# Optimization experiments

Measured on AMD Instinct MI355X. Metric: run time of the kernel, lower is better.

Reference implementation:

```python
import jax, jax.numpy as jnp
import numpy as np

B, S, D, H = 4, 2048, 1024, 16
DH = D // H  # 64
NEG_INF = jnp.float32(-1e30)


def setup_inputs() -> dict:
    key = jax.random.key(0)
    ks = jax.random.split(key, 11)
    s = 0.02
    inp = {
        "query": jax.random.normal(ks[0], (B, S, D), jnp.float32),
        "key":   jax.random.normal(ks[1], (B, S, D), jnp.float32),
        "value": jax.random.normal(ks[2], (B, S, D), jnp.float32),
        # causal mask, broadcastable to [B,H,Sq,Sk]; 0 -> masked
        "mask": jnp.tril(jnp.ones((S, S), jnp.int32))[None, None, :, :],
        "Wq": jax.random.normal(ks[3], (D, D), jnp.float32) * s,
        "bq": jnp.zeros((D,), jnp.float32),
        "Wk": jax.random.normal(ks[4], (D, D), jnp.float32) * s,
        "bk": jnp.zeros((D,), jnp.float32),
        "Wv": jax.random.normal(ks[5], (D, D), jnp.float32) * s,
        "bv": jnp.zeros((D,), jnp.float32),
        "Wo": jax.random.normal(ks[6], (D, D), jnp.float32) * s,
        "bo": jnp.zeros((D,), jnp.float32),
    }
    return inp


def _heads(x):
    # [B,S,D] -> [B,H,S,DH]
    b, s, _ = x.shape
    return x.reshape(b, s, H, DH).transpose(0, 2, 1, 3)


def reference(query, key, value, mask, Wq, bq, Wk, bk, Wv, bv, Wo, bo):
    q = _heads(query @ Wq.T + bq)   # [B,H,S,DH]
    k = _heads(key   @ Wk.T + bk)
    v = _heads(value @ Wv.T + bv)
    scale = 1.0 / jnp.sqrt(jnp.float32(DH))
    logits = jnp.einsum('bhqd,bhkd->bhqk', q, k) * scale  # [B,H,S,S]
    logits = jnp.where(mask == 0, NEG_INF, logits)
    attn = jax.nn.softmax(logits, axis=-1)
    out = jnp.einsum('bhqk,bhkd->bhqd', attn, v)          # [B,H,S,DH]
    out = out.transpose(0, 2, 1, 3).reshape(query.shape[0], query.shape[1], D)
    return out @ Wo.T + bo
```

## Files before the change

### kernel.cpp

```cpp
#include <hip/hip_runtime.h>
#include <hip/hip_bf16.h>
#include <stdint.h>

#define BB 4
#define SS 2048
#define DD 1024
#define HH 16
#define DHH 64

typedef __attribute__((ext_vector_type(8))) short short8_t;
typedef __attribute__((ext_vector_type(4))) short short4_t;
typedef __attribute__((ext_vector_type(4))) float f32x4;
typedef unsigned short u16;

static __device__ __forceinline__ u16 f2bf(float x) {
    uint32_t u = __float_as_uint(x);
    u += 0x7fffu + ((u >> 16) & 1u);
    return (u16)(u >> 16);
}

static __device__ __forceinline__ void gload16(const void* g, void* l) {
    __builtin_amdgcn_global_load_lds((const __attribute__((address_space(1))) void*)g,
                                     (__attribute__((address_space(3))) void*)l, 16, 0, 0);
}

__global__ __launch_bounds__(256) void convert_x3(
    const float* __restrict__ a, const float* __restrict__ b, const float* __restrict__ c,
    u16* __restrict__ oa, u16* __restrict__ ob, u16* __restrict__ oc)
{
    const float* s; u16* d;
    if (blockIdx.z == 0)      { s = a; d = oa; }
    else if (blockIdx.z == 1) { s = b; d = ob; }
    else                      { s = c; d = oc; }
    size_t i = ((size_t)blockIdx.x * 256 + threadIdx.x) * 8;
    f32x4 v0 = *(const f32x4*)(s + i);
    f32x4 v1 = *(const f32x4*)(s + i + 4);
    short8_t o;
#pragma unroll
    for (int j = 0; j < 4; j++) { o[j] = (short)f2bf(v0[j]); o[4 + j] = (short)f2bf(v1[j]); }
    *(short8_t*)(d + i) = o;
}

__global__ __launch_bounds__(256) void convert_w4(
    const float* __restrict__ a, const float* __restrict__ b,
    const float* __restrict__ c, const float* __restrict__ dd_,
    u16* __restrict__ oa, u16* __restrict__ ob, u16* __restrict__ oc, u16* __restrict__ od)
{
    const float* s; u16* d;
    if (blockIdx.z == 0)      { s = a;   d = oa; }
    else if (blockIdx.z == 1) { s = b;   d = ob; }
    else if (blockIdx.z == 2) { s = c;   d = oc; }
    else                      { s = dd_; d = od; }
    size_t i = ((size_t)blockIdx.x * 256 + threadIdx.x) * 8;
    f32x4 v0 = *(const f32x4*)(s + i);
    f32x4 v1 = *(const f32x4*)(s + i + 4);
    short8_t o;
#pragma unroll
    for (int j = 0; j < 4; j++) { o[j] = (short)f2bf(v0[j]); o[4 + j] = (short)f2bf(v1[j]); }
    *(short8_t*)(d + i) = o;
}

template<int OMODE>
__global__ __launch_bounds__(256) void gemm_v3(
    const u16* __restrict__ A, const u16* __restrict__ B,
    const float* __restrict__ bias, void* __restrict__ outp)
{
    __shared__ u16 As[128 * 64];
    __shared__ u16 Bs[128 * 64];

    const int tid = threadIdx.x;
    const int lane = tid & 63;
    const int w  = tid >> 6;
    const int wr = w >> 1, wc = w & 1;
    const int g  = lane >> 4, c = lane & 15;
    const int cs7 = c & 7;

    const int m0 = blockIdx.x * 128;
    const int n0 = blockIdx.y * 128;

    f32x4 acc[4][4] = {};

    const int srow  = w * 32 + (lane >> 3);
    const int sslot = (lane & 7) ^ (srow & 7);
    const u16* aSrc = A + (size_t)(m0 + srow) * DD + sslot * 8;
    const u16* bSrc = B + (size_t)(n0 + srow) * DD + sslot * 8;

    for (int ks = 0; ks < 16; ks++) {
        __syncthreads();
#pragma unroll
        for (int j = 0; j < 4; j++) {
            gload16(aSrc + (size_t)j * 8 * DD + ks * 64, &As[(w * 32 + j * 8) * 64]);
            gload16(bSrc + (size_t)j * 8 * DD + ks * 64, &Bs[(w * 32 + j * 8) * 64]);
        }
        __syncthreads();

#pragma unroll
        for (int kc = 0; kc < 2; kc++) {
            const int rdoff = ((kc * 4 + g) ^ cs7) * 8;
            short8_t af[4], bfr[4];
#pragma unroll
            for (int m = 0; m < 4; m++)
                af[m] = *(const short8_t*)&As[(wr * 64 + m * 16 + c) * 64 + rdoff];
#pragma unroll
            for (int n = 0; n < 4; n++)
                bfr[n] = *(const short8_t*)&Bs[(wc * 64 + n * 16 + c) * 64 + rdoff];
#pragma unroll
            for (int m = 0; m < 4; m++)
#pragma unroll
                for (int n = 0; n < 4; n++)
                    acc[m][n] = __builtin_amdgcn_mfma_f32_16x16x32_bf16(af[m], bfr[n], acc[m][n], 0, 0, 0);
        }
    }

    if (OMODE == 0) {
        u16* out = (u16*)outp;
#pragma unroll
        for (int m = 0; m < 4; m++)
#pragma unroll
            for (int n = 0; n < 4; n++) {
                const int gn = n0 + wc * 64 + n * 16 + c;
                const int h = gn >> 6, dh = gn & 63;
                const float bv_ = bias[gn];
#pragma unroll
                for (int i = 0; i < 4; i++) {
                    const int gm = m0 + wr * 64 + m * 16 + g * 4 + i;
                    const int b = gm >> 11, s = gm & (SS - 1);
                    out[(((size_t)(b * HH + h)) * SS + s) * DHH + dh] = f2bf(acc[m][n][i] + bv_);
                }
            }
    } else if (OMODE == 1) {
        u16* out = (u16*)outp;
#pragma unroll
        for (int m = 0; m < 4; m++)
#pragma unroll
            for (int n = 0; n < 4; n++) {
                const int gn = n0 + wc * 64 + n * 16 + c;
                const int h = gn >> 6, dh = gn & 63;
                const float bv_ = bias[gn];
                const int gm0 = m0 + wr * 64 + m * 16 + g * 4;
                const int b = gm0 >> 11, s = gm0 & (SS - 1);
                short4_t pk;
#pragma unroll
                for (int i = 0; i < 4; i++) pk[i] = (short)f2bf(acc[m][n][i] + bv_);
                *(short4_t*)&out[(((size_t)(b * HH + h)) * DHH + dh) * SS + s] = pk;
            }
    } else {
        float* out = (float*)outp;
#pragma unroll
        for (int m = 0; m < 4; m++)
#pragma unroll
            for (int n = 0; n < 4; n++) {
                const int gn = n0 + wc * 64 + n * 16 + c;
                const float bv_ = bias[gn];
#pragma unroll
                for (int i = 0; i < 4; i++) {
                    const int gm = m0 + wr * 64 + m * 16 + g * 4 + i;
                    out[(size_t)gm * DD + gn] = acc[m][n][i] + bv_;
                }
            }
    }
}

__global__ __launch_bounds__(256) void attn_v3(
    const u16* __restrict__ qb, const u16* __restrict__ kb,
    const u16* __restrict__ vtb, u16* __restrict__ attb)
{
    __shared__ u16 Kt[64 * 64];
    __shared__ u16 Vt[64 * 64];
    __shared__ u16 Pb[4][32 * 64];

    const int tid = threadIdx.x;
    const int lane = tid & 63;
    const int w = tid >> 6;
    const int g = lane >> 4, c = lane & 15;
    const int cs7 = c & 7;
    const int qt = 15 - blockIdx.x;
    const int bh = blockIdx.y;
    const size_t base = (size_t)bh * SS * DHH;
    const int qw = qt * 128 + w * 32;

    short8_t qa[2][2];
#pragma unroll
    for (int fr = 0; fr < 2; fr++)
#pragma unroll
        for (int kc = 0; kc < 2; kc++)
            qa[fr][kc] = *(const short8_t*)(qb + base + (size_t)(qw + fr * 16 + c) * DHH + kc * 32 + g * 8);

    f32x4 o[2][4] = {};
    float lp[2] = {0.f, 0.f};

    const int NT = 2 * qt + 2;
    const int sr = tid >> 2;
    const int s4 = (tid & 3) * 16;
    const int swz = (sr & 7) << 3;
    const u16* kpb = kb  + base + (size_t)sr * DHH + s4;
    const u16* vpb = vtb + base + (size_t)sr * SS + s4;

    short8_t kr0 = *(const short8_t*)(kpb);
    short8_t kr1 = *(const short8_t*)(kpb + 8);
    short8_t vr0 = *(const short8_t*)(vpb);
    short8_t vr1 = *(const short8_t*)(vpb + 8);

    for (int t = 0; t < NT; ++t) {
        __syncthreads();
        *(short8_t*)&Kt[sr * 64 + (s4 ^ swz)]       = kr0;
        *(short8_t*)&Kt[sr * 64 + ((s4 + 8) ^ swz)] = kr1;
        *(short8_t*)&Vt[sr * 64 + (s4 ^ swz)]       = vr0;
        *(short8_t*)&Vt[sr * 64 + ((s4 + 8) ^ swz)] = vr1;
        __syncthreads();

        if (t + 1 < NT) {
            kr0 = *(const short8_t*)(kpb + (size_t)(t + 1) * 64 * DHH);
            kr1 = *(const short8_t*)(kpb + (size_t)(t + 1) * 64 * DHH + 8);
            vr0 = *(const short8_t*)(vpb + (t + 1) * 64);
            vr1 = *(const short8_t*)(vpb + (t + 1) * 64 + 8);
        }

        const int k0g = t * 64;
        const bool act0 = (k0g <= qw + 15);
        const bool act1 = (k0g <= qw + 31);

        f32x4 sacc[2][4] = {};
#pragma unroll
        for (int n = 0; n < 4; n++) {
            const int krow = n * 16 + c;
            const int ksw = (krow & 7) << 3;
#pragma unroll
            for (int kc = 0; kc < 2; kc++) {
                short8_t kf = *(const short8_t*)&Kt[krow * 64 + ((kc * 32 + g * 8) ^ ksw)];
                if (act0) sacc[0][n] = __builtin_amdgcn_mfma_f32_16x16x32_bf16(kf, qa[0][kc], sacc[0][n], 0, 0, 0);
                if (act1) sacc[1][n] = __builtin_amdgcn_mfma_f32_16x16x32_bf16(kf, qa[1][kc], sacc[1][n], 0, 0, 0);
            }
        }

        const bool diag = (k0g + 63 > qw);
#pragma unroll
        for (int fr = 0; fr < 2; fr++) {
            if (fr == 0 ? !act0 : !act1) continue;
            const int qq = qw + fr * 16 + c;
            float e[4][4];
            float ls = 0.f;
#pragma unroll
            for (int n = 0; n < 4; n++) {
                const int kbse = k0g + n * 16 + 4 * g;
#pragma unroll
                for (int i = 0; i < 4; i++) {
                    float pv = exp2f(sacc[fr][n][i] * 0.18033688f);
                    if (diag && (kbse + i > qq)) pv = 0.f;
                    e[n][i] = pv;
                    ls += pv;
                }
            }
            lp[fr] += ls;
            const int prow = (fr * 16 + c) * 64;
#pragma unroll
            for (int n = 0; n < 4; n++)
#pragma unroll
                for (int hi = 0; hi < 2; hi++) {
                    uint32_t pk = (__float_as_uint(e[n][2 * hi]) >> 16) |
                                  (__float_as_uint(e[n][2 * hi + 1]) & 0xFFFF0000u);
                    *(uint32_t*)&Pb[w][prow + (((2 * n + (g >> 1)) ^ cs7) * 8 + 4 * (g & 1) + 2 * hi)] = pk;
                }
        }

        short8_t pa[2][2];
        if (act0) {
            const int prow = c * 64;
            pa[0][0] = *(const short8_t*)&Pb[w][prow + ((g ^ cs7) * 8)];
            pa[0][1] = *(const short8_t*)&Pb[w][prow + (((4 + g) ^ cs7) * 8)];
        }
        if (act1) {
            const int prow = (16 + c) * 64;
            pa[1][0] = *(const short8_t*)&Pb[w][prow + ((g ^ cs7) * 8)];
            pa[1][1] = *(const short8_t*)&Pb[w][prow + (((4 + g) ^ cs7) * 8)];
        }

#pragma unroll
        for (int n2 = 0; n2 < 4; n2++) {
            const int vrow = n2 * 16 + c;
            const int vsw = (vrow & 7) << 3;
#pragma unroll
            for (int kc = 0; kc < 2; kc++) {
                short8_t vf = *(const short8_t*)&Vt[vrow * 64 + ((kc * 32 + g * 8) ^ vsw)];
                if (act0) o[0][n2] = __builtin_amdgcn_mfma_f32_16x16x32_bf16(pa[0][kc], vf, o[0][n2], 0, 0, 0);
                if (act1) o[1][n2] = __builtin_amdgcn_mfma_f32_16x16x32_bf16(pa[1][kc], vf, o[1][n2], 0, 0, 0);
            }
        }
    }

    const int b_ = bh >> 4, h_ = bh & 15;
#pragma unroll
    for (int fr = 0; fr < 2; fr++) {
        float l = lp[fr];
        l += __shfl_xor(l, 16, 64);
        l += __shfl_xor(l, 32, 64);
#pragma unroll
        for (int i = 0; i < 4; i++) {
            const float li = __shfl(l, g * 4 + i, 16);
            const float inv = 1.0f / li;
            const int qg = qw + fr * 16 + g * 4 + i;
            const size_t obase = ((size_t)b_ * SS + qg) * DD + h_ * DHH;
#pragma unroll
            for (int n2 = 0; n2 < 4; n2++)
                attb[obase + n2 * 16 + c] = f2bf(o[fr][n2][i] * inv);
        }
    }
}

extern "C" void kernel_launch(void* const* d_in, const int* in_sizes, int n_in,
                              void* d_out, int out_size, void* d_ws, size_t ws_size,
                              hipStream_t stream) {
    const float* query = (const float*)d_in[0];
    const float* key_  = (const float*)d_in[1];
    const float* value = (const float*)d_in[2];
    const float* Wq = (const float*)d_in[4];
    const float* bq = (const float*)d_in[5];
    const float* Wk = (const float*)d_in[6];
    const float* bk = (const float*)d_in[7];
    const float* Wv = (const float*)d_in[8];
    const float* bv = (const float*)d_in[9];
    const float* Wo = (const float*)d_in[10];
    const float* bo = (const float*)d_in[11];
    float* out = (float*)d_out;

    u16* ws = (u16*)d_ws;
    const size_t N  = (size_t)BB * SS * DD;
    const size_t WN = (size_t)DD * DD;

    u16* s0 = ws;
    u16* s1 = ws + N;
    u16* s2 = ws + 2 * N;
    u16* s3 = ws + 3 * N;
    u16* w4 = ws + 4 * N;

    dim3 blk(256);
    convert_x3<<<dim3(4096, 1, 3), blk, 0, stream>>>(query, key_, value, s0, s1, s2);
    convert_w4<<<dim3(512, 1, 4), blk, 0, stream>>>(Wq, Wk, Wv, Wo,
                                                    w4, w4 + WN, w4 + 2 * WN, w4 + 3 * WN);
    gemm_v3<0><<<dim3(64, 8), blk, 0, stream>>>(s1, w4 + WN,     bk, s3);
    gemm_v3<1><<<dim3(64, 8), blk, 0, stream>>>(s2, w4 + 2 * WN, bv, s1);
    gemm_v3<0><<<dim3(64, 8), blk, 0, stream>>>(s0, w4,          bq, s2);
    attn_v3<<<dim3(16, 64), blk, 0, stream>>>(s2, s3, s1, s0);
    gemm_v3<2><<<dim3(64, 8), blk, 0, stream>>>(s0, w4 + 3 * WN, bo, out);
}
```

Measured before the change: 410.9 us.

## Read K/V fragments directly from global memory in attention and merge convert kernels

The attention kernel no longer stages K and V tiles through shared memory with two barriers per tile. Each wave now loads its MFMA fragments straight from global memory, relying on L1/L2 for reuse across the four waves, and raises wave priority around the MFMA loops. The input and weight conversion kernels are merged into one launch, with early exit for the smaller weight slices. The cost is redundant global/cache traffic, since each wave fetches the same K/V data, and load latency is no longer hidden by software prefetch.

```diff
diff --git a/kernel.cpp b/kernel.cpp
--- a/kernel.cpp
+++ b/kernel.cpp
@@ -24,33 +24,25 @@
                                      (__attribute__((address_space(3))) void*)l, 16, 0, 0);
 }
 
-__global__ __launch_bounds__(256) void convert_x3(
-    const float* __restrict__ a, const float* __restrict__ b, const float* __restrict__ c,
-    u16* __restrict__ oa, u16* __restrict__ ob, u16* __restrict__ oc)
+__global__ __launch_bounds__(256) void convert_all(
+    const float* __restrict__ x0, const float* __restrict__ x1, const float* __restrict__ x2,
+    const float* __restrict__ w0, const float* __restrict__ w1,
+    const float* __restrict__ w2, const float* __restrict__ w3,
+    u16* __restrict__ ox0, u16* __restrict__ ox1, u16* __restrict__ ox2,
+    u16* __restrict__ ow0, u16* __restrict__ ow1, u16* __restrict__ ow2, u16* __restrict__ ow3)
 {
+    const int y = blockIdx.y;
+    if (y >= 3 && blockIdx.x >= 512) return;
     const float* s; u16* d;
-    if (blockIdx.z == 0)      { s = a; d = oa; }
-    else if (blockIdx.z == 1) { s = b; d = ob; }
-    else                      { s = c; d = oc; }
-    size_t i = ((size_t)blockIdx.x * 256 + threadIdx.x) * 8;
-    f32x4 v0 = *(const f32x4*)(s + i);
-    f32x4 v1 = *(const f32x4*)(s + i + 4);
-    short8_t o;
-#pragma unroll
-    for (int j = 0; j < 4; j++) { o[j] = (short)f2bf(v0[j]); o[4 + j] = (short)f2bf(v1[j]); }
-    *(short8_t*)(d + i) = o;
-}
-
-__global__ __launch_bounds__(256) void convert_w4(
-    const float* __restrict__ a, const float* __restrict__ b,
-    const float* __restrict__ c, const float* __restrict__ dd_,
-    u16* __restrict__ oa, u16* __restrict__ ob, u16* __restrict__ oc, u16* __restrict__ od)
-{
-    const float* s; u16* d;
-    if (blockIdx.z == 0)      { s = a;   d = oa; }
-    else if (blockIdx.z == 1) { s = b;   d = ob; }
-    else if (blockIdx.z == 2) { s = c;   d = oc; }
-    else                      { s = dd_; d = od; }
+    switch (y) {
+        case 0: s = x0; d = ox0; break;
+        case 1: s = x1; d = ox1; break;
+        case 2: s = x2; d = ox2; break;
+        case 3: s = w0; d = ow0; break;
+        case 4: s = w1; d = ow1; break;
+        case 5: s = w2; d = ow2; break;
+        default: s = w3; d = ow3; break;
+    }
     size_t i = ((size_t)blockIdx.x * 256 + threadIdx.x) * 8;
     f32x4 v0 = *(const f32x4*)(s + i);
     f32x4 v1 = *(const f32x4*)(s + i + 4);
@@ -161,12 +153,10 @@
     }
 }
 
-__global__ __launch_bounds__(256) void attn_v3(
+__global__ __launch_bounds__(256) void attn_v4(
     const u16* __restrict__ qb, const u16* __restrict__ kb,
     const u16* __restrict__ vtb, u16* __restrict__ attb)
 {
-    __shared__ u16 Kt[64 * 64];
-    __shared__ u16 Vt[64 * 64];
     __shared__ u16 Pb[4][32 * 64];
 
     const int tid = threadIdx.x;
@@ -190,48 +180,27 @@
     float lp[2] = {0.f, 0.f};
 
     const int NT = 2 * qt + 2;
-    const int sr = tid >> 2;
-    const int s4 = (tid & 3) * 16;
-    const int swz = (sr & 7) << 3;
-    const u16* kpb = kb  + base + (size_t)sr * DHH + s4;
-    const u16* vpb = vtb + base + (size_t)sr * SS + s4;
-
-    short8_t kr0 = *(const short8_t*)(kpb);
-    short8_t kr1 = *(const short8_t*)(kpb + 8);
-    short8_t vr0 = *(const short8_t*)(vpb);
-    short8_t vr1 = *(const short8_t*)(vpb + 8);
+    const u16* kB = kb + base;
+    const u16* vB = vtb + base;
 
     for (int t = 0; t < NT; ++t) {
-        __syncthreads();
-        *(short8_t*)&Kt[sr * 64 + (s4 ^ swz)]       = kr0;
-        *(short8_t*)&Kt[sr * 64 + ((s4 + 8) ^ swz)] = kr1;
-        *(short8_t*)&Vt[sr * 64 + (s4 ^ swz)]       = vr0;
-        *(short8_t*)&Vt[sr * 64 + ((s4 + 8) ^ swz)] = vr1;
-        __syncthreads();
-
-        if (t + 1 < NT) {
-            kr0 = *(const short8_t*)(kpb + (size_t)(t + 1) * 64 * DHH);
-            kr1 = *(const short8_t*)(kpb + (size_t)(t + 1) * 64 * DHH + 8);
-            vr0 = *(const short8_t*)(vpb + (t + 1) * 64);
-            vr1 = *(const short8_t*)(vpb + (t + 1) * 64 + 8);
-        }
-
         const int k0g = t * 64;
         const bool act0 = (k0g <= qw + 15);
         const bool act1 = (k0g <= qw + 31);
 
         f32x4 sacc[2][4] = {};
+        __builtin_amdgcn_s_setprio(1);
 #pragma unroll
         for (int n = 0; n < 4; n++) {
-            const int krow = n * 16 + c;
-            const int ksw = (krow & 7) << 3;
+            const u16* kr = kB + (size_t)(k0g + n * 16 + c) * DHH;
 #pragma unroll
             for (int kc = 0; kc < 2; kc++) {
-                short8_t kf = *(const short8_t*)&Kt[krow * 64 + ((kc * 32 + g * 8) ^ ksw)];
+                short8_t kf = *(const short8_t*)(kr + kc * 32 + g * 8);
                 if (act0) sacc[0][n] = __builtin_amdgcn_mfma_f32_16x16x32_bf16(kf, qa[0][kc], sacc[0][n], 0, 0, 0);
                 if (act1) sacc[1][n] = __builtin_amdgcn_mfma_f32_16x16x32_bf16(kf, qa[1][kc], sacc[1][n], 0, 0, 0);
             }
         }
+        __builtin_amdgcn_s_setprio(0);
 
         const bool diag = (k0g + 63 > qw);
 #pragma unroll
@@ -275,17 +244,18 @@
             pa[1][1] = *(const short8_t*)&Pb[w][prow + (((4 + g) ^ cs7) * 8)];
         }
 
+        __builtin_amdgcn_s_setprio(1);
 #pragma unroll
         for (int n2 = 0; n2 < 4; n2++) {
-            const int vrow = n2 * 16 + c;
-            const int vsw = (vrow & 7) << 3;
+            const u16* vr = vB + (size_t)(n2 * 16 + c) * SS + k0g;
 #pragma unroll
             for (int kc = 0; kc < 2; kc++) {
-                short8_t vf = *(const short8_t*)&Vt[vrow * 64 + ((kc * 32 + g * 8) ^ vsw)];
+                short8_t vf = *(const short8_t*)(vr + kc * 32 + g * 8);
                 if (act0) o[0][n2] = __builtin_amdgcn_mfma_f32_16x16x32_bf16(pa[0][kc], vf, o[0][n2], 0, 0, 0);
                 if (act1) o[1][n2] = __builtin_amdgcn_mfma_f32_16x16x32_bf16(pa[1][kc], vf, o[1][n2], 0, 0, 0);
             }
         }
+        __builtin_amdgcn_s_setprio(0);
     }
 
     const int b_ = bh >> 4, h_ = bh & 15;
@@ -334,12 +304,12 @@
     u16* w4 = ws + 4 * N;
 
     dim3 blk(256);
-    convert_x3<<<dim3(4096, 1, 3), blk, 0, stream>>>(query, key_, value, s0, s1, s2);
-    convert_w4<<<dim3(512, 1, 4), blk, 0, stream>>>(Wq, Wk, Wv, Wo,
-                                                    w4, w4 + WN, w4 + 2 * WN, w4 + 3 * WN);
+    convert_all<<<dim3(4096, 7), blk, 0, stream>>>(query, key_, value, Wq, Wk, Wv, Wo,
+                                                   s0, s1, s2,
+                                                   w4, w4 + WN, w4 + 2 * WN, w4 + 3 * WN);
     gemm_v3<0><<<dim3(64, 8), blk, 0, stream>>>(s1, w4 + WN,     bk, s3);
     gemm_v3<1><<<dim3(64, 8), blk, 0, stream>>>(s2, w4 + 2 * WN, bv, s1);
     gemm_v3<0><<<dim3(64, 8), blk, 0, stream>>>(s0, w4,          bq, s2);
-    attn_v3<<<dim3(16, 64), blk, 0, stream>>>(s2, s3, s1, s0);
+    attn_v4<<<dim3(16, 64), blk, 0, stream>>>(s2, s3, s1, s0);
     gemm_v3<2><<<dim3(64, 8), blk, 0, stream>>>(s0, w4 + 3 * WN, bo, out);
 }
```

Measured after the change: 629.0 us. +53.1%, slower.
